# Kernel tuning notes

Measured on AMD Instinct MI355X. Metric: run time of the kernel, lower is better.

## Reference

```python
import jax, jax.numpy as jnp
import numpy as np

TS = 6      # texture cube size (hard-coded in module)
S = 256     # image size (NMR default / ref image size)
DIST = 2.732


def _look_at(verts, eye):
    # NMR look_at: camera at eye, looking at origin, up=(0,1,0)
    eye = jnp.asarray(eye, verts.dtype)
    z = -eye / jnp.linalg.norm(eye)
    up = jnp.array([0.0, 1.0, 0.0], verts.dtype)
    x = jnp.cross(up, z)
    x = x / jnp.linalg.norm(x)
    y = jnp.cross(z, x)
    R = jnp.stack([x, y, z])          # rows = camera axes
    return (verts - eye) @ R.T


def _render(verts, faces, tex_flat, eye):
    # verts [V,3], faces [F,3] int, tex_flat [F*TS^3, 3] (tanh already applied)
    v = _look_at(verts, eye)
    fv = v[faces]                      # [F,3,3]
    p0, p1, p2 = fv[:, 0], fv[:, 1], fv[:, 2]
    ps = (2.0 * jnp.arange(S, dtype=verts.dtype) + 1.0 - S) / S
    PX = jnp.broadcast_to(ps[None, :], (S, S)).reshape(-1)      # x right
    PY = jnp.broadcast_to(-ps[:, None], (S, S)).reshape(-1)     # y up (row 0 = top)

    def edge(a, b):
        # signed edge function, [F,HW]
        return ((PX[None, :] - a[:, 0:1]) * (b[:, 1:2] - a[:, 1:2])
                - (PY[None, :] - a[:, 1:2]) * (b[:, 0:1] - a[:, 0:1]))

    e0 = edge(p1, p2)
    e1 = edge(p2, p0)
    e2 = edge(p0, p1)
    # per-face signed area (double area) [F,1]
    area = ((p1[:, 0] - p0[:, 0]) * (p2[:, 1] - p0[:, 1])
            - (p1[:, 1] - p0[:, 1]) * (p2[:, 0] - p0[:, 0]))[:, None]
    ok = jnp.abs(area) > 1e-8
    inv = jnp.where(ok, 1.0 / jnp.where(ok, area, 1.0), 0.0)
    w0, w1, w2 = e0 * inv, e1 * inv, e2 * inv            # barycentric weights
    inside = (w0 >= 0) & (w1 >= 0) & (w2 >= 0) & ok       # both windings (fill_back)
    z = w0 * p0[:, 2:3] + w1 * p1[:, 2:3] + w2 * p2[:, 2:3]
    depth = jnp.where(inside & (z > 0), z, jnp.inf)       # z-buffer candidates
    best = jnp.argmin(depth, axis=0)                      # [HW] winning face
    hit = jnp.take_along_axis(depth, best[None, :], axis=0)[0] < jnp.inf
    wb = jnp.stack([jnp.take_along_axis(w, best[None, :], axis=0)[0]
                    for w in (w0, w1, w2)], axis=-1)       # [HW,3]
    ti = jnp.clip(jnp.round(wb * (TS - 1)), 0, TS - 1).astype(jnp.int32)
    flat = ((best * TS + ti[:, 0]) * TS + ti[:, 1]) * TS + ti[:, 2]
    colors = tex_flat[flat]                                # [HW,3] gather
    img = jnp.where(hit[:, None], colors, 0.0)
    return img.reshape(S, S, 3).transpose(2, 0, 1)[None]   # [1,3,S,S]


def setup_inputs() -> dict:
    key = jax.random.key(0)
    k1, k2, k3, k4, k5 = jax.random.split(key, 5)
    V, F = 252, 500
    return {
        "vertices": jax.random.normal(k1, (1, V, 3), jnp.float32),
        "faces": jax.random.randint(k2, (1, F, 3), 0, V, jnp.int64),
        "textures": jax.random.normal(k3, (1, F, TS, TS, TS, 3), jnp.float32),
        "image_ref": jax.random.uniform(k4, (1, 3, S, S), jnp.float32),
        "image_ref_2": jax.random.uniform(k5, (1, 3, S, S), jnp.float32),
    }


def reference(vertices, faces, textures, image_ref, image_ref_2):
    tex_flat = jnp.tanh(textures[0]).reshape(-1, 3)
    v, f = vertices[0], faces[0]
    # eye = get_points_from_angles(2.732, 180, 0) -> (0, 0, +d)
    img1 = _render(v, f, tex_flat, jnp.array([0.0, 0.0, DIST], jnp.float32))
    loss_one_side = jnp.sum((img1 - image_ref) ** 2)
    # eye = get_points_from_angles(2.732, 0, 0) -> (0, 0, -d)
    img2 = _render(v, f, tex_flat, jnp.array([0.0, 0.0, -DIST], jnp.float32))
    loss_symmetric = jnp.sum((img2 - image_ref_2) ** 2)
    return (loss_one_side + loss_symmetric) / 2
```

## Files before the change

### kernel.cpp

```cpp
#include <hip/hip_runtime.h>
#include <math.h>

#define IMG_S 256
#define NPIX (IMG_S * IMG_S)
#define NFACE 500
#define NCHUNK 16
#define FPC 32
#define PPT 8
#define TSZ 6
#define DIST 2.732f

struct FaceCoef {
    float A0, B0, C0, A1, B1, C1, A2, B2, C2, Az, Bz, Cz;
};

__device__ __forceinline__ void edge_coef(float ax, float ay, float bx, float by,
                                          float inv, float& A, float& B, float& C) {
    float dy = by - ay;
    float dx = bx - ax;
    A = dy * inv;
    B = -dx * inv;
    C = (ay * dx - ax * dy) * inv;
}

__device__ __forceinline__ bool compute_face_bbox(const float* __restrict__ verts,
                                                  const int* __restrict__ faces,
                                                  int f, int view, FaceCoef& fc,
                                                  float& ymin, float& ymax, float& zmax) {
    int i0 = faces[f * 3 + 0];
    int i1 = faces[f * 3 + 1];
    int i2 = faces[f * 3 + 2];

    float v0x = verts[i0 * 3 + 0], v0y = verts[i0 * 3 + 1], v0z = verts[i0 * 3 + 2];
    float v1x = verts[i1 * 3 + 0], v1y = verts[i1 * 3 + 1], v1z = verts[i1 * 3 + 2];
    float v2x = verts[i2 * 3 + 0], v2y = verts[i2 * 3 + 1], v2z = verts[i2 * 3 + 2];

    float p0x, p0y, p0z, p1x, p1y, p1z, p2x, p2y, p2z;
    if (view == 0) {
        p0x = -v0x; p0y = v0y; p0z = DIST - v0z;
        p1x = -v1x; p1y = v1y; p1z = DIST - v1z;
        p2x = -v2x; p2y = v2y; p2z = DIST - v2z;
    } else {
        p0x = v0x; p0y = v0y; p0z = v0z + DIST;
        p1x = v1x; p1y = v1y; p1z = v1z + DIST;
        p2x = v2x; p2y = v2y; p2z = v2z + DIST;
    }

    ymin = fminf(p0y, fminf(p1y, p2y));
    ymax = fmaxf(p0y, fmaxf(p1y, p2y));
    zmax = fmaxf(p0z, fmaxf(p1z, p2z));

    float area = (p1x - p0x) * (p2y - p0y) - (p1y - p0y) * (p2x - p0x);
    bool ok = fabsf(area) > 1e-8f;
    if (!ok) return false;

    float inv = 1.0f / area;
    edge_coef(p1x, p1y, p2x, p2y, inv, fc.A0, fc.B0, fc.C0);
    edge_coef(p2x, p2y, p0x, p0y, inv, fc.A1, fc.B1, fc.C1);
    edge_coef(p0x, p0y, p1x, p1y, inv, fc.A2, fc.B2, fc.C2);
    fc.Az = fc.A0 * p0z + fc.A1 * p1z + fc.A2 * p2z;
    fc.Bz = fc.B0 * p0z + fc.B1 * p1z + fc.B2 * p2z;
    fc.Cz = fc.C0 * p0z + fc.C1 * p1z + fc.C2 * p2z;
    return true;
}

__device__ __forceinline__ float pix_x(int ix) {
    return (2.0f * (float)ix + 1.0f - (float)IMG_S) * (1.0f / (float)IMG_S);
}
__device__ __forceinline__ float pix_y(int iy) {
    return -((2.0f * (float)iy + 1.0f - (float)IMG_S) * (1.0f / (float)IMG_S));
}

__global__ __launch_bounds__(256) void raster_chunk_kernel(
    const float* __restrict__ verts,
    const int*   __restrict__ faces,
    unsigned long long* __restrict__ zbuf)
{
    __shared__ float4 sc[FPC][3];
    __shared__ int    sidx[FPC];
    __shared__ int    scount;

    const int tile  = blockIdx.x;
    const int chunk = blockIdx.y;
    const int view  = blockIdx.z;
    const int fbase = chunk * FPC;

    const float py_top = pix_y(tile * PPT);
    const float py_bot = pix_y(tile * PPT + PPT - 1);

    if (threadIdx.x < 64) {
        bool keep = false;
        FaceCoef c;
        int fi = fbase + (int)threadIdx.x;
        if ((int)threadIdx.x < FPC && fi < NFACE) {
            float ymin, ymax, zmax;
            bool ok = compute_face_bbox(verts, faces, fi, view, c, ymin, ymax, zmax);
            keep = ok && (ymax >= py_bot) && (ymin <= py_top) && (zmax > 0.0f);
        }
        unsigned long long bal = __ballot(keep);
        int pos = __popcll(bal & ((1ull << (threadIdx.x & 63)) - 1ull));
        if (keep) {
            sc[pos][0] = make_float4(c.A0, c.B0, c.C0, c.A1);
            sc[pos][1] = make_float4(c.B1, c.C1, c.A2, c.B2);
            sc[pos][2] = make_float4(c.C2, c.Az, c.Bz, c.Cz);
            sidx[pos] = fi;
        }
        if (threadIdx.x == 0) scount = (int)__popcll(bal);
    }
    __syncthreads();
    const int cnt = scount;

    const int ix = threadIdx.x;
    const float px = pix_x(ix);
    float py[PPT];
    #pragma unroll
    for (int k = 0; k < PPT; ++k) py[k] = pix_y(tile * PPT + k);

    float bestz[PPT];
    int   bestj[PPT];
    #pragma unroll
    for (int k = 0; k < PPT; ++k) { bestz[k] = INFINITY; bestj[k] = -1; }

    for (int j = 0; j < cnt; ++j) {
        float4 q0 = sc[j][0];
        float4 q1 = sc[j][1];
        float4 q2 = sc[j][2];
        float d0 = fmaf(px, q0.x, q0.z);
        float d1 = fmaf(px, q0.w, q1.y);
        float d2 = fmaf(px, q1.z, q2.x);
        float dz = fmaf(px, q2.y, q2.w);
        #pragma unroll
        for (int k = 0; k < PPT; ++k) {
            float w0 = fmaf(q0.y, py[k], d0);
            float w1 = fmaf(q1.x, py[k], d1);
            float w2 = fmaf(q1.w, py[k], d2);
            float z  = fmaf(q2.z, py[k], dz);
            float wmin = fminf(w0, fminf(w1, w2));
            float s = fminf(z, bestz[k] - z);
            bool cc = (wmin >= 0.0f) && (s > 0.0f);
            bestz[k] = cc ? z : bestz[k];
            bestj[k] = cc ? j : bestj[k];
        }
    }

    unsigned long long* __restrict__ zb = zbuf + (size_t)view * NPIX;
    #pragma unroll
    for (int k = 0; k < PPT; ++k) {
        if (bestj[k] >= 0) {
            unsigned long long packed =
                ((unsigned long long)__float_as_uint(bestz[k]) << 32) |
                (unsigned int)sidx[bestj[k]];
            atomicMin(&zb[(tile * PPT + k) * IMG_S + ix], packed);
        }
    }
}

__global__ __launch_bounds__(256) void shade_loss_kernel(
    const float* __restrict__ verts,
    const int*   __restrict__ faces,
    const float* __restrict__ tex,
    const float* __restrict__ ref0,
    const float* __restrict__ ref1,
    const unsigned long long* __restrict__ zbuf,
    float* __restrict__ out)
{
    __shared__ float red[4];
    const int gid  = blockIdx.x * blockDim.x + threadIdx.x;
    const int view = gid >> 16;
    const int pix  = gid & (NPIX - 1);

    unsigned long long best = zbuf[(size_t)view * NPIX + pix];

    float c0 = 0.0f, c1 = 0.0f, c2 = 0.0f;
    if (best != ~0ull) {
        int fidx = (int)(best & 0xFFFFFFFFu);
        FaceCoef fcw;
        float ymin, ymax, zmax;
        compute_face_bbox(verts, faces, fidx, view, fcw, ymin, ymax, zmax);
        const float px = pix_x(pix & (IMG_S - 1));
        const float py = pix_y(pix >> 8);
        float w0 = fmaf(fcw.B0, py, fmaf(px, fcw.A0, fcw.C0));
        float w1 = fmaf(fcw.B1, py, fmaf(px, fcw.A1, fcw.C1));
        float w2 = fmaf(fcw.B2, py, fmaf(px, fcw.A2, fcw.C2));
        int t0 = (int)fminf(fmaxf(rintf(w0 * (float)(TSZ - 1)), 0.0f), (float)(TSZ - 1));
        int t1 = (int)fminf(fmaxf(rintf(w1 * (float)(TSZ - 1)), 0.0f), (float)(TSZ - 1));
        int t2 = (int)fminf(fmaxf(rintf(w2 * (float)(TSZ - 1)), 0.0f), (float)(TSZ - 1));
        int flat = ((fidx * TSZ + t0) * TSZ + t1) * TSZ + t2;
        const float* t = tex + (long)flat * 3;
        c0 = tanhf(t[0]);
        c1 = tanhf(t[1]);
        c2 = tanhf(t[2]);
    }

    const float* __restrict__ ref = (view == 0) ? ref0 : ref1;
    float d0 = c0 - ref[0 * NPIX + pix];
    float d1 = c1 - ref[1 * NPIX + pix];
    float d2 = c2 - ref[2 * NPIX + pix];
    float acc = fmaf(d0, d0, fmaf(d1, d1, d2 * d2));

    for (int off = 32; off > 0; off >>= 1)
        acc += __shfl_down(acc, off, 64);
    int lane = threadIdx.x & 63;
    int wid = threadIdx.x >> 6;
    if (lane == 0) red[wid] = acc;
    __syncthreads();
    if (threadIdx.x == 0)
        atomicAdd(out, 0.5f * (red[0] + red[1] + red[2] + red[3]));
}

extern "C" void kernel_launch(void* const* d_in, const int* in_sizes, int n_in,
                              void* d_out, int out_size, void* d_ws, size_t ws_size,
                              hipStream_t stream) {
    const float* verts = (const float*)d_in[0];
    const int*   faces = (const int*)d_in[1];
    const float* tex   = (const float*)d_in[2];
    const float* ref0  = (const float*)d_in[3];
    const float* ref1  = (const float*)d_in[4];
    float* out = (float*)d_out;

    unsigned long long* zbuf = (unsigned long long*)d_ws;

    hipMemsetAsync(zbuf, 0xFF, (size_t)2 * NPIX * sizeof(unsigned long long), stream);
    hipMemsetAsync(out, 0, sizeof(float), stream);

    dim3 grid1(NPIX / (256 * PPT), NCHUNK, 2);
    raster_chunk_kernel<<<grid1, 256, 0, stream>>>(verts, faces, zbuf);

    const int shade_blocks = (2 * NPIX) / 256;
    shade_loss_kernel<<<shade_blocks, 256, 0, stream>>>(verts, faces, tex, ref0, ref1,
                                                        zbuf, out);
}
```

Baseline: 87.95 us.

## Replace atomic z-buffer with per-chunk depth planes reduced in shading kernel

Each raster block now writes its per-pixel packed depth/face result to its own plane instead of doing 64-bit atomicMin on a shared z-buffer. The shading kernel takes the minimum across the chunk planes. This removes both memset launches; the loss accumulator is zeroed inside the raster kernel. Chunks grow to 64 faces each (8 chunks), so the whole first wavefront evaluates faces. The cost is more workspace traffic, 8 planes per view written and read back, in exchange for no atomics and fewer launches.

```diff
diff --git a/kernel.cpp b/kernel.cpp
--- a/kernel.cpp
+++ b/kernel.cpp
@@ -4,8 +4,8 @@
 #define IMG_S 256
 #define NPIX (IMG_S * IMG_S)
 #define NFACE 500
-#define NCHUNK 16
-#define FPC 32
+#define NCHUNK 8
+#define FPC 64
 #define PPT 8
 #define TSZ 6
 #define DIST 2.732f
@@ -74,7 +74,8 @@
 __global__ __launch_bounds__(256) void raster_chunk_kernel(
     const float* __restrict__ verts,
     const int*   __restrict__ faces,
-    unsigned long long* __restrict__ zbuf)
+    unsigned long long* __restrict__ planes,
+    float* __restrict__ out)
 {
     __shared__ float4 sc[FPC][3];
     __shared__ int    sidx[FPC];
@@ -85,6 +86,9 @@
     const int view  = blockIdx.z;
     const int fbase = chunk * FPC;
 
+    if (blockIdx.x == 0 && blockIdx.y == 0 && blockIdx.z == 0 && threadIdx.x == 0)
+        out[0] = 0.0f;
+
     const float py_top = pix_y(tile * PPT);
     const float py_bot = pix_y(tile * PPT + PPT - 1);
 
@@ -92,7 +96,7 @@
         bool keep = false;
         FaceCoef c;
         int fi = fbase + (int)threadIdx.x;
-        if ((int)threadIdx.x < FPC && fi < NFACE) {
+        if (fi < NFACE) {
             float ymin, ymax, zmax;
             bool ok = compute_face_bbox(verts, faces, fi, view, c, ymin, ymax, zmax);
             keep = ok && (ymax >= py_bot) && (ymin <= py_top) && (zmax > 0.0f);
@@ -143,15 +147,15 @@
         }
     }
 
-    unsigned long long* __restrict__ zb = zbuf + (size_t)view * NPIX;
+    unsigned long long* __restrict__ outp =
+        planes + (size_t)(view * NCHUNK + chunk) * NPIX + tile * (PPT * IMG_S) + ix;
     #pragma unroll
     for (int k = 0; k < PPT; ++k) {
-        if (bestj[k] >= 0) {
-            unsigned long long packed =
-                ((unsigned long long)__float_as_uint(bestz[k]) << 32) |
-                (unsigned int)sidx[bestj[k]];
-            atomicMin(&zb[(tile * PPT + k) * IMG_S + ix], packed);
-        }
+        unsigned long long packed = ~0ull;
+        if (bestj[k] >= 0)
+            packed = ((unsigned long long)__float_as_uint(bestz[k]) << 32) |
+                     (unsigned int)sidx[bestj[k]];
+        outp[k * IMG_S] = packed;
     }
 }
 
@@ -161,7 +165,7 @@
     const float* __restrict__ tex,
     const float* __restrict__ ref0,
     const float* __restrict__ ref1,
-    const unsigned long long* __restrict__ zbuf,
+    const unsigned long long* __restrict__ planes,
     float* __restrict__ out)
 {
     __shared__ float red[4];
@@ -169,7 +173,13 @@
     const int view = gid >> 16;
     const int pix  = gid & (NPIX - 1);
 
-    unsigned long long best = zbuf[(size_t)view * NPIX + pix];
+    const unsigned long long* p = planes + (size_t)view * NCHUNK * NPIX + pix;
+    unsigned long long best = p[0];
+    #pragma unroll
+    for (int c = 1; c < NCHUNK; ++c) {
+        unsigned long long v = p[(size_t)c * NPIX];
+        best = (v < best) ? v : best;
+    }
 
     float c0 = 0.0f, c1 = 0.0f, c2 = 0.0f;
     if (best != ~0ull) {
@@ -218,15 +228,12 @@
     const float* ref1  = (const float*)d_in[4];
     float* out = (float*)d_out;
 
-    unsigned long long* zbuf = (unsigned long long*)d_ws;
-
-    hipMemsetAsync(zbuf, 0xFF, (size_t)2 * NPIX * sizeof(unsigned long long), stream);
-    hipMemsetAsync(out, 0, sizeof(float), stream);
+    unsigned long long* planes = (unsigned long long*)d_ws;
 
     dim3 grid1(NPIX / (256 * PPT), NCHUNK, 2);
-    raster_chunk_kernel<<<grid1, 256, 0, stream>>>(verts, faces, zbuf);
+    raster_chunk_kernel<<<grid1, 256, 0, stream>>>(verts, faces, planes, out);
 
     const int shade_blocks = (2 * NPIX) / 256;
     shade_loss_kernel<<<shade_blocks, 256, 0, stream>>>(verts, faces, tex, ref0, ref1,
-                                                        zbuf, out);
-}
+                                                        planes, out);
+}
```

Measured after the change: 88.95 us. Within noise of the previous version (+1.1%).
